# Kernel tuning notes

Measured on AMD Instinct MI355X. Metric: run time of the kernel, lower is better.

The kernel has to match this reference:

```python
import jax, jax.numpy as jnp
import numpy as np
import math

D_MODEL = 512
NHEAD = 8
D_K = D_MODEL // NHEAD
WINDOW = 128
BATCH = 1
SEQ = 4096
NEG = -1e9  # matches torch masked_fill value


def setup_inputs() -> dict:
    key = jax.random.key(0)
    ks = jax.random.split(key, 9)
    s = 1.0 / math.sqrt(D_MODEL)
    return {
        "x": jax.random.normal(ks[0], (BATCH, SEQ, D_MODEL), dtype=jnp.float32),
        "wq": jax.random.uniform(ks[1], (D_MODEL, D_MODEL), jnp.float32, -s, s),
        "bq": jax.random.uniform(ks[2], (D_MODEL,), jnp.float32, -s, s),
        "wk": jax.random.uniform(ks[3], (D_MODEL, D_MODEL), jnp.float32, -s, s),
        "bk": jax.random.uniform(ks[4], (D_MODEL,), jnp.float32, -s, s),
        "wv": jax.random.uniform(ks[5], (D_MODEL, D_MODEL), jnp.float32, -s, s),
        "bv": jax.random.uniform(ks[6], (D_MODEL,), jnp.float32, -s, s),
        "wo": jax.random.uniform(ks[7], (D_MODEL, D_MODEL), jnp.float32, -s, s),
        "bo": jax.random.uniform(ks[8], (D_MODEL,), jnp.float32, -s, s),
    }


def reference(x, wq, bq, wk, bk, wv, bv, wo, bo):
    B, S, D = x.shape
    # projections -> (B, H, S, d_k)
    q = (x @ wq.T + bq).reshape(B, S, NHEAD, D_K).transpose(0, 2, 1, 3)
    k = (x @ wk.T + bk).reshape(B, S, NHEAD, D_K).transpose(0, 2, 1, 3)
    v = (x @ wv.T + bv).reshape(B, S, NHEAD, D_K).transpose(0, 2, 1, 3)
    # dense scores, band-masked (faithful to original: full S x S)
    scores = jnp.einsum('bhqd,bhkd->bhqk', q, k) / math.sqrt(D_K)
    idx = jnp.arange(S)
    band = jnp.abs(idx[:, None] - idx[None, :]) <= WINDOW  # (S, S)
    scores = jnp.where(band[None, None], scores, NEG)
    attn = jax.nn.softmax(scores, axis=-1)  # (B, H, S, S)
    ctx = jnp.einsum('bhqk,bhkd->bhqd', attn, v)
    ctx = ctx.transpose(0, 2, 1, 3).reshape(B, S, D)
    out = ctx @ wo.T + bo
    return out, attn
```

## Files before the change

kernel.cpp:

```cpp
#include <hip/hip_runtime.h>
#include <hip/hip_bf16.h>
#include <math.h>

#define S 4096
#define D 512
#define H 8
#define DK 64
#define WIN 128

typedef __attribute__((ext_vector_type(8))) short bf16x8;
typedef __attribute__((ext_vector_type(4))) float f32x4;

__device__ __forceinline__ unsigned short f2bf(float f) {
    __hip_bfloat16 h = __float2bfloat16(f);
    return *(unsigned short*)&h;
}

__global__ __launch_bounds__(256) void conv_bf16_kernel(
    const float* __restrict__ x,
    const float* __restrict__ wq, const float* __restrict__ wk,
    const float* __restrict__ wv, const float* __restrict__ wo,
    unsigned short* __restrict__ xb,
    unsigned short* __restrict__ wqb, unsigned short* __restrict__ wkb,
    unsigned short* __restrict__ wvb, unsigned short* __restrict__ wob)
{
    const float* src; unsigned short* dst; int n;
    switch (blockIdx.y) {
        case 0:  src = x;  dst = xb;  n = S * D; break;
        case 1:  src = wq; dst = wqb; n = D * D; break;
        case 2:  src = wk; dst = wkb; n = D * D; break;
        case 3:  src = wv; dst = wvb; n = D * D; break;
        default: src = wo; dst = wob; n = D * D; break;
    }
    const int i = (blockIdx.x * 256 + threadIdx.x) * 8;
    if (i >= n) return;
    float4 a = *(const float4*)&src[i];
    float4 b = *(const float4*)&src[i + 4];
    ushort4 o0 = {f2bf(a.x), f2bf(a.y), f2bf(a.z), f2bf(a.w)};
    ushort4 o1 = {f2bf(b.x), f2bf(b.y), f2bf(b.z), f2bf(b.w)};
    *(ushort4*)&dst[i]     = o0;
    *(ushort4*)&dst[i + 4] = o1;
}

__global__ __launch_bounds__(256) void vtrans_kernel(
    const unsigned short* __restrict__ vb, unsigned short* __restrict__ vT)
{
    __shared__ unsigned short T[64][72];
    const int tid = threadIdx.x;
    const int s0 = blockIdx.x * 64;
    const int h  = blockIdx.y;
    const int r = tid >> 2;
    const int c = (tid & 3) * 16;
    *(bf16x8*)&T[r][c]     = *(const bf16x8*)&vb[(size_t)(s0 + r) * 512 + h * 64 + c];
    *(bf16x8*)&T[r][c + 8] = *(const bf16x8*)&vb[(size_t)(s0 + r) * 512 + h * 64 + c + 8];
    __syncthreads();
    unsigned short o[16];
    #pragma unroll
    for (int e = 0; e < 16; ++e) o[e] = T[c + e][r];
    unsigned short* dst = &vT[((size_t)h * 64 + r) * 4096 + s0 + c];
    *(bf16x8*)&dst[0] = *(bf16x8*)&o[0];
    *(bf16x8*)&dst[8] = *(bf16x8*)&o[8];
}

__device__ __forceinline__ void mfma_gemm_body(
    const unsigned short* __restrict__ A,
    const unsigned short* __restrict__ W16,
    const float* __restrict__ bias,
    float* __restrict__ C,
    unsigned short* __restrict__ CB)
{
    __shared__ unsigned short Bs[64][520];

    const int tid  = threadIdx.x;
    const int m0   = blockIdx.x * 128;
    const int n0   = blockIdx.y * 64;
    const int wv   = tid >> 6;
    const int lane = tid & 63;
    const int l16  = lane & 15;
    const int klo  = (lane >> 4) * 8;

    #pragma unroll
    for (int it = 0; it < 16; ++it) {
        const int c   = tid + it * 256;
        const int row = c >> 6;
        const int kc  = (c & 63) * 8;
        *(bf16x8*)&Bs[row][kc] =
            *(const bf16x8*)&W16[(size_t)(n0 + row) * 512 + kc];
    }
    __syncthreads();

    const unsigned short* arow0 = &A[(size_t)(m0 + wv * 32 + l16) * 512 + klo];
    const unsigned short* arow1 = arow0 + 16 * 512;

    f32x4 acc[2][4];
    #pragma unroll
    for (int r = 0; r < 2; ++r)
        #pragma unroll
        for (int nf = 0; nf < 4; ++nf)
            acc[r][nf] = (f32x4){0.f, 0.f, 0.f, 0.f};

    #pragma unroll 4
    for (int kb = 0; kb < 512; kb += 32) {
        bf16x8 a0 = *(const bf16x8*)&arow0[kb];
        bf16x8 a1 = *(const bf16x8*)&arow1[kb];
        #pragma unroll
        for (int nf = 0; nf < 4; ++nf) {
            bf16x8 b = *(const bf16x8*)&Bs[nf * 16 + l16][kb + klo];
            acc[0][nf] = __builtin_amdgcn_mfma_f32_16x16x32_bf16(a0, b, acc[0][nf], 0, 0, 0);
            acc[1][nf] = __builtin_amdgcn_mfma_f32_16x16x32_bf16(a1, b, acc[1][nf], 0, 0, 0);
        }
    }

    const int r0 = (lane >> 4) * 4;
    #pragma unroll
    for (int r = 0; r < 2; ++r) {
        #pragma unroll
        for (int nf = 0; nf < 4; ++nf) {
            const int col = n0 + nf * 16 + l16;
            const float bb = bias[col];
            #pragma unroll
            for (int vv = 0; vv < 4; ++vv) {
                const int row = m0 + wv * 32 + r * 16 + r0 + vv;
                const float val = acc[r][nf][vv] + bb;
                if (C)  C [(size_t)row * 512 + col] = val;
                if (CB) CB[(size_t)row * 512 + col] = f2bf(val);
            }
        }
    }
}

__global__ __launch_bounds__(256) void proj3_kernel(
    const unsigned short* __restrict__ xb,
    const unsigned short* __restrict__ wqb, const float* __restrict__ bq,
    const unsigned short* __restrict__ wkb, const float* __restrict__ bk,
    const unsigned short* __restrict__ wvb, const float* __restrict__ bv,
    unsigned short* __restrict__ qb, unsigned short* __restrict__ kb,
    unsigned short* __restrict__ vb)
{
    const unsigned short* W; const float* b; unsigned short* CB;
    if (blockIdx.z == 0)      { W = wqb; b = bq; CB = qb; }
    else if (blockIdx.z == 1) { W = wkb; b = bk; CB = kb; }
    else                      { W = wvb; b = bv; CB = vb; }
    mfma_gemm_body(xb, W, b, nullptr, CB);
}

__global__ __launch_bounds__(256) void outproj_kernel(
    const unsigned short* __restrict__ ctxb,
    const unsigned short* __restrict__ wob, const float* __restrict__ bo,
    float* __restrict__ out)
{
    mfma_gemm_body(ctxb, wob, bo, out, nullptr);
}

__global__ __launch_bounds__(256) void band_attn_kernel(
    const unsigned short* __restrict__ qb, const unsigned short* __restrict__ kb,
    const unsigned short* __restrict__ vT,
    float* __restrict__ attn, unsigned short* __restrict__ ctxb)
{
    __shared__ __align__(16) unsigned short KV[64][72];
    __shared__ float P[16][336];
    __shared__ float rinvs[16];

    const int tid = threadIdx.x;
    const int h  = blockIdx.y;
    const int q0 = blockIdx.x * 16;
    const int w0 = q0 - 128;

    const int wv   = tid >> 6;
    const int lane = tid & 63;
    const int l16  = lane & 15;
    const int klo  = (lane >> 4) * 8;
    const int r0   = (lane >> 4) * 4;

    const unsigned short* qrow = &qb[(size_t)(q0 + l16) * 512 + h * 64 + klo];
    const bf16x8 aq0 = *(const bf16x8*)&qrow[0];
    const bf16x8 aq1 = *(const bf16x8*)&qrow[32];

    const int lr = tid >> 2;
    const int ld = (tid & 3) * 16;

    for (int ch = 0; ch < 5; ++ch) {
        const int c0 = w0 + ch * 64;
        if (c0 + 64 <= 0 || c0 >= S) continue;
        __syncthreads();
        {
            const int krow = min(max(c0 + lr, 0), S - 1);
            const unsigned short* src = &kb[(size_t)krow * 512 + h * 64 + ld];
            *(bf16x8*)&KV[lr][ld]     = *(const bf16x8*)&src[0];
            *(bf16x8*)&KV[lr][ld + 8] = *(const bf16x8*)&src[8];
        }
        __syncthreads();

        f32x4 acc = (f32x4){0.f, 0.f, 0.f, 0.f};
        bf16x8 b0 = *(const bf16x8*)&KV[wv * 16 + l16][klo];
        bf16x8 b1 = *(const bf16x8*)&KV[wv * 16 + l16][32 + klo];
        acc = __builtin_amdgcn_mfma_f32_16x16x32_bf16(aq0, b0, acc, 0, 0, 0);
        acc = __builtin_amdgcn_mfma_f32_16x16x32_bf16(aq1, b1, acc, 0, 0, 0);
        #pragma unroll
        for (int vv = 0; vv < 4; ++vv)
            P[r0 + vv][ch * 64 + wv * 16 + l16] = acc[vv] * 0.125f;
    }
    __syncthreads();

    {
        const int r   = tid >> 4;
        const int lx  = tid & 15;
        const int i   = q0 + r;
        const int lo = max(i - WIN, 0) - w0;
        const int hi = min(i + WIN, S - 1) - w0;

        float m = -1e30f;
        for (int c = lo + lx; c <= hi; c += 16) m = fmaxf(m, P[r][c]);
        m = fmaxf(m, __shfl_xor(m, 1));
        m = fmaxf(m, __shfl_xor(m, 2));
        m = fmaxf(m, __shfl_xor(m, 4));
        m = fmaxf(m, __shfl_xor(m, 8));

        float sum = 0.f;
        for (int c = lx; c < 320; c += 16) {
            float e = 0.f;
            if (c >= lo && c <= hi) {
                e = __expf(P[r][c] - m);
                sum += e;
            }
            P[r][c] = e;
        }
        sum += __shfl_xor(sum, 1);
        sum += __shfl_xor(sum, 2);
        sum += __shfl_xor(sum, 4);
        sum += __shfl_xor(sum, 8);
        if (lx == 0) rinvs[r] = 1.0f / sum;
    }

    f32x4 pacc = (f32x4){0.f, 0.f, 0.f, 0.f};
    const int dd = tid >> 2;
    const int sc = (tid & 3) * 16;
    const unsigned short* vtd = &vT[((size_t)h * 64 + dd) * 4096];
    for (int ch = 0; ch < 5; ++ch) {
        const int c0 = w0 + ch * 64;
        if (c0 + 64 <= 0 || c0 >= S) continue;
        __syncthreads();
        {
            const int offs = min(max(c0 + sc, 0), S - 16);
            *(bf16x8*)&KV[dd][sc]     = *(const bf16x8*)&vtd[offs];
            *(bf16x8*)&KV[dd][sc + 8] = *(const bf16x8*)&vtd[offs + 8];
        }
        __syncthreads();

        #pragma unroll
        for (int kk = 0; kk < 64; kk += 32) {
            f32x4 p0 = *(const f32x4*)&P[l16][ch * 64 + kk + klo];
            f32x4 p1 = *(const f32x4*)&P[l16][ch * 64 + kk + klo + 4];
            unsigned short ab[8] = {f2bf(p0[0]), f2bf(p0[1]), f2bf(p0[2]), f2bf(p0[3]),
                                    f2bf(p1[0]), f2bf(p1[1]), f2bf(p1[2]), f2bf(p1[3])};
            bf16x8 a = *(const bf16x8*)ab;
            bf16x8 b = *(const bf16x8*)&KV[wv * 16 + l16][kk + klo];
            pacc = __builtin_amdgcn_mfma_f32_16x16x32_bf16(a, b, pacc, 0, 0, 0);
        }
    }

    #pragma unroll
    for (int vv = 0; vv < 4; ++vv) {
        const int row = q0 + r0 + vv;
        ctxb[(size_t)row * 512 + h * 64 + wv * 16 + l16] =
            f2bf(pacc[vv] * rinvs[r0 + vv]);
    }

    float* rowbase = attn + (size_t)h * S * S;
    #pragma unroll 1
    for (int r = 0; r < 16; ++r) {
        const int i = q0 + r;
        float* rowp = rowbase + (size_t)i * S;
        const int lo = max(i - WIN, 0) - w0;
        const int hi = min(i + WIN, S - 1) - w0;
        const float rv = rinvs[r];
        #pragma unroll
        for (int t = 0; t < 4; ++t) {
            const int c4 = (tid + t * 256) << 2;
            const int lc = c4 - w0;
            float4 o;
            if (lc >= lo && lc + 3 <= hi) {
                float4 p = *(const float4*)&P[r][lc];
                o.x = p.x * rv; o.y = p.y * rv; o.z = p.z * rv; o.w = p.w * rv;
            } else if (lc + 3 < lo || lc > hi) {
                o = make_float4(0.f, 0.f, 0.f, 0.f);
            } else {
                o.x = (lc + 0 >= lo && lc + 0 <= hi) ? P[r][lc + 0] * rv : 0.f;
                o.y = (lc + 1 >= lo && lc + 1 <= hi) ? P[r][lc + 1] * rv : 0.f;
                o.z = (lc + 2 >= lo && lc + 2 <= hi) ? P[r][lc + 2] * rv : 0.f;
                o.w = (lc + 3 >= lo && lc + 3 <= hi) ? P[r][lc + 3] * rv : 0.f;
            }
            *(float4*)&rowp[c4] = o;
        }
    }
}

extern "C" void kernel_launch(void* const* d_in, const int* in_sizes, int n_in,
                              void* d_out, int out_size, void* d_ws, size_t ws_size,
                              hipStream_t stream)
{
    (void)in_sizes; (void)n_in; (void)out_size; (void)ws_size;
    const float* x  = (const float*)d_in[0];
    const float* wq = (const float*)d_in[1];
    const float* bq = (const float*)d_in[2];
    const float* wk = (const float*)d_in[3];
    const float* bk = (const float*)d_in[4];
    const float* wv = (const float*)d_in[5];
    const float* bv = (const float*)d_in[6];
    const float* wo = (const float*)d_in[7];
    const float* bo = (const float*)d_in[8];

    float* out  = (float*)d_out;
    float* attn = out + (size_t)S * D;

    unsigned short* xb   = (unsigned short*)d_ws;
    unsigned short* qb   = xb   + (size_t)S * D;
    unsigned short* kb   = qb   + (size_t)S * D;
    unsigned short* vb   = kb   + (size_t)S * D;
    unsigned short* ctxb = vb   + (size_t)S * D;
    unsigned short* vT   = ctxb + (size_t)S * D;
    unsigned short* wqb  = vT   + (size_t)S * D;
    unsigned short* wkb  = wqb  + (size_t)D * D;
    unsigned short* wvb  = wkb  + (size_t)D * D;
    unsigned short* wob  = wvb  + (size_t)D * D;

    conv_bf16_kernel<<<dim3(1024, 5), 256, 0, stream>>>(
        x, wq, wk, wv, wo, xb, wqb, wkb, wvb, wob);
    proj3_kernel<<<dim3(32, 8, 3), 256, 0, stream>>>(
        xb, wqb, bq, wkb, bk, wvb, bv, qb, kb, vb);
    vtrans_kernel<<<dim3(64, 8), 256, 0, stream>>>(vb, vT);
    band_attn_kernel<<<dim3(256, 8), 256, 0, stream>>>(qb, kb, vT, attn, ctxb);
    outproj_kernel<<<dim3(32, 8), 256, 0, stream>>>(ctxb, wob, bo, out);
}
```

Before: 148.3 us.

## Fuse V transpose into projection epilogue and halve GEMM shared tile

The V projection now writes its bf16 output directly in transposed (head-dim major) layout from the GEMM epilogue, which removes the separate vtrans kernel launch and the round trip through the vb buffer. The GEMM body also stages the weight tile in two K-halves of 256 instead of the full 512, cutting shared memory per block to raise occupancy. The cost is extra barriers and less weight reuse per load phase, and the transposed stores are 8-byte scattered writes with a 4096-element stride.

```diff
diff --git a/kernel.cpp b/kernel.cpp
--- a/kernel.cpp
+++ b/kernel.cpp
@@ -42,34 +42,15 @@
     *(ushort4*)&dst[i + 4] = o1;
 }
 
-__global__ __launch_bounds__(256) void vtrans_kernel(
-    const unsigned short* __restrict__ vb, unsigned short* __restrict__ vT)
-{
-    __shared__ unsigned short T[64][72];
-    const int tid = threadIdx.x;
-    const int s0 = blockIdx.x * 64;
-    const int h  = blockIdx.y;
-    const int r = tid >> 2;
-    const int c = (tid & 3) * 16;
-    *(bf16x8*)&T[r][c]     = *(const bf16x8*)&vb[(size_t)(s0 + r) * 512 + h * 64 + c];
-    *(bf16x8*)&T[r][c + 8] = *(const bf16x8*)&vb[(size_t)(s0 + r) * 512 + h * 64 + c + 8];
-    __syncthreads();
-    unsigned short o[16];
-    #pragma unroll
-    for (int e = 0; e < 16; ++e) o[e] = T[c + e][r];
-    unsigned short* dst = &vT[((size_t)h * 64 + r) * 4096 + s0 + c];
-    *(bf16x8*)&dst[0] = *(bf16x8*)&o[0];
-    *(bf16x8*)&dst[8] = *(bf16x8*)&o[8];
-}
-
 __device__ __forceinline__ void mfma_gemm_body(
     const unsigned short* __restrict__ A,
     const unsigned short* __restrict__ W16,
     const float* __restrict__ bias,
     float* __restrict__ C,
-    unsigned short* __restrict__ CB)
-{
-    __shared__ unsigned short Bs[64][520];
+    unsigned short* __restrict__ CB,
+    unsigned short* __restrict__ CBT)
+{
+    __shared__ unsigned short Bs[64][264];
 
     const int tid  = threadIdx.x;
     const int m0   = blockIdx.x * 128;
@@ -79,16 +60,6 @@
     const int l16  = lane & 15;
     const int klo  = (lane >> 4) * 8;
 
-    #pragma unroll
-    for (int it = 0; it < 16; ++it) {
-        const int c   = tid + it * 256;
-        const int row = c >> 6;
-        const int kc  = (c & 63) * 8;
-        *(bf16x8*)&Bs[row][kc] =
-            *(const bf16x8*)&W16[(size_t)(n0 + row) * 512 + kc];
-    }
-    __syncthreads();
-
     const unsigned short* arow0 = &A[(size_t)(m0 + wv * 32 + l16) * 512 + klo];
     const unsigned short* arow1 = arow0 + 16 * 512;
 
@@ -99,16 +70,31 @@
         for (int nf = 0; nf < 4; ++nf)
             acc[r][nf] = (f32x4){0.f, 0.f, 0.f, 0.f};
 
-    #pragma unroll 4
-    for (int kb = 0; kb < 512; kb += 32) {
-        bf16x8 a0 = *(const bf16x8*)&arow0[kb];
-        bf16x8 a1 = *(const bf16x8*)&arow1[kb];
-        #pragma unroll
-        for (int nf = 0; nf < 4; ++nf) {
-            bf16x8 b = *(const bf16x8*)&Bs[nf * 16 + l16][kb + klo];
-            acc[0][nf] = __builtin_amdgcn_mfma_f32_16x16x32_bf16(a0, b, acc[0][nf], 0, 0, 0);
-            acc[1][nf] = __builtin_amdgcn_mfma_f32_16x16x32_bf16(a1, b, acc[1][nf], 0, 0, 0);
-        }
+    #pragma unroll
+    for (int half = 0; half < 2; ++half) {
+        const int kbase = half * 256;
+        #pragma unroll
+        for (int it = 0; it < 8; ++it) {
+            const int c   = tid + it * 256;
+            const int row = c >> 5;
+            const int kc  = (c & 31) * 8;
+            *(bf16x8*)&Bs[row][kc] =
+                *(const bf16x8*)&W16[(size_t)(n0 + row) * 512 + kbase + kc];
+        }
+        __syncthreads();
+
+        #pragma unroll 4
+        for (int kb = 0; kb < 256; kb += 32) {
+            bf16x8 a0 = *(const bf16x8*)&arow0[kbase + kb];
+            bf16x8 a1 = *(const bf16x8*)&arow1[kbase + kb];
+            #pragma unroll
+            for (int nf = 0; nf < 4; ++nf) {
+                bf16x8 b = *(const bf16x8*)&Bs[nf * 16 + l16][kb + klo];
+                acc[0][nf] = __builtin_amdgcn_mfma_f32_16x16x32_bf16(a0, b, acc[0][nf], 0, 0, 0);
+                acc[1][nf] = __builtin_amdgcn_mfma_f32_16x16x32_bf16(a1, b, acc[1][nf], 0, 0, 0);
+            }
+        }
+        __syncthreads();
     }
 
     const int r0 = (lane >> 4) * 4;
@@ -118,12 +104,22 @@
         for (int nf = 0; nf < 4; ++nf) {
             const int col = n0 + nf * 16 + l16;
             const float bb = bias[col];
-            #pragma unroll
-            for (int vv = 0; vv < 4; ++vv) {
-                const int row = m0 + wv * 32 + r * 16 + r0 + vv;
-                const float val = acc[r][nf][vv] + bb;
-                if (C)  C [(size_t)row * 512 + col] = val;
-                if (CB) CB[(size_t)row * 512 + col] = f2bf(val);
+            if (CBT) {
+                ushort4 o;
+                o.x = f2bf(acc[r][nf][0] + bb);
+                o.y = f2bf(acc[r][nf][1] + bb);
+                o.z = f2bf(acc[r][nf][2] + bb);
+                o.w = f2bf(acc[r][nf][3] + bb);
+                const int row0 = m0 + wv * 32 + r * 16 + r0;
+                *(ushort4*)&CBT[(size_t)col * 4096 + row0] = o;
+            } else {
+                #pragma unroll
+                for (int vv = 0; vv < 4; ++vv) {
+                    const int row = m0 + wv * 32 + r * 16 + r0 + vv;
+                    const float val = acc[r][nf][vv] + bb;
+                    if (C)  C [(size_t)row * 512 + col] = val;
+                    if (CB) CB[(size_t)row * 512 + col] = f2bf(val);
+                }
             }
         }
     }
@@ -135,13 +131,14 @@
     const unsigned short* __restrict__ wkb, const float* __restrict__ bk,
     const unsigned short* __restrict__ wvb, const float* __restrict__ bv,
     unsigned short* __restrict__ qb, unsigned short* __restrict__ kb,
-    unsigned short* __restrict__ vb)
-{
-    const unsigned short* W; const float* b; unsigned short* CB;
-    if (blockIdx.z == 0)      { W = wqb; b = bq; CB = qb; }
-    else if (blockIdx.z == 1) { W = wkb; b = bk; CB = kb; }
-    else                      { W = wvb; b = bv; CB = vb; }
-    mfma_gemm_body(xb, W, b, nullptr, CB);
+    unsigned short* __restrict__ vT)
+{
+    if (blockIdx.z == 0)
+        mfma_gemm_body(xb, wqb, bq, nullptr, qb, nullptr);
+    else if (blockIdx.z == 1)
+        mfma_gemm_body(xb, wkb, bk, nullptr, kb, nullptr);
+    else
+        mfma_gemm_body(xb, wvb, bv, nullptr, nullptr, vT);
 }
 
 __global__ __launch_bounds__(256) void outproj_kernel(
@@ -149,7 +146,7 @@
     const unsigned short* __restrict__ wob, const float* __restrict__ bo,
     float* __restrict__ out)
 {
-    mfma_gemm_body(ctxb, wob, bo, out, nullptr);
+    mfma_gemm_body(ctxb, wob, bo, out, nullptr, nullptr);
 }
 
 __global__ __launch_bounds__(256) void band_attn_kernel(
@@ -316,8 +313,7 @@
     unsigned short* xb   = (unsigned short*)d_ws;
     unsigned short* qb   = xb   + (size_t)S * D;
     unsigned short* kb   = qb   + (size_t)S * D;
-    unsigned short* vb   = kb   + (size_t)S * D;
-    unsigned short* ctxb = vb   + (size_t)S * D;
+    unsigned short* ctxb = kb   + (size_t)S * D;
     unsigned short* vT   = ctxb + (size_t)S * D;
     unsigned short* wqb  = vT   + (size_t)S * D;
     unsigned short* wkb  = wqb  + (size_t)D * D;
@@ -327,8 +323,7 @@
     conv_bf16_kernel<<<dim3(1024, 5), 256, 0, stream>>>(
         x, wq, wk, wv, wo, xb, wqb, wkb, wvb, wob);
     proj3_kernel<<<dim3(32, 8, 3), 256, 0, stream>>>(
-        xb, wqb, bq, wkb, bk, wvb, bv, qb, kb, vb);
-    vtrans_kernel<<<dim3(64, 8), 256, 0, stream>>>(vb, vT);
+        xb, wqb, bq, wkb, bk, wvb, bv, qb, kb, vT);
     band_attn_kernel<<<dim3(256, 8), 256, 0, stream>>>(qb, kb, vT, attn, ctxb);
     outproj_kernel<<<dim3(32, 8), 256, 0, stream>>>(ctxb, wob, bo, out);
 }
```

New measurement: 148.0 us. About the same (-0.2%).
